# Performance work log

Measured on AMD Instinct MI355X. Metric: run time of the kernel, lower is better.

## Reference

```python
import jax, jax.numpy as jnp
import numpy as np

EMBED_DIM = 64
CODEBOOK_SIZE = 2048
COMMITMENT_COST = 1.0


def setup_inputs() -> dict:
    key = jax.random.key(0)
    k1, k2 = jax.random.split(key)
    inputs = jax.random.normal(k1, (32, 2048, EMBED_DIM), dtype=jnp.float32)
    embeddings = jax.random.normal(k2, (EMBED_DIM, CODEBOOK_SIZE), dtype=jnp.float32)
    return {"inputs": inputs, "embeddings": embeddings}


def reference(inputs, embeddings):
    # inference path (training=False): deterministic argmin quantization.
    D = embeddings.shape[0]
    K = embeddings.shape[1]
    flat = inputs.reshape(-1, D)                       # [N, D]
    similarity = flat @ embeddings                     # [N, K]
    distances = (jnp.sum(flat * flat, axis=1, keepdims=True)
                 - 2.0 * similarity
                 + jnp.sum(embeddings * embeddings, axis=0, keepdims=True))
    # gumbel layer with temperature 0 / eval mode -> argmax(-dist) == argmin(dist)
    flat_indices = jnp.argmax(-distances, axis=1)      # [N]
    encodings = jax.nn.one_hot(flat_indices, K, dtype=jnp.float32)  # [N, K]
    encoding_indices = flat_indices.reshape(inputs.shape[:-1])      # [B, T]
    quantized = jnp.take(embeddings.T, encoding_indices, axis=0)    # [B, T, D]
    e_latent_loss = jnp.mean(jnp.square(jax.lax.stop_gradient(quantized) - inputs))
    loss = e_latent_loss * COMMITMENT_COST
    return quantized, encodings, encoding_indices, loss
```

## Files before the change

### kernel.cpp

```cpp
#include <hip/hip_runtime.h>

#define N_ROWS 65536
#define DDIM   64
#define KCODES 2048
#define NB     128
#define TAU    0.05f

#define Q_OFF    ((size_t)0)
#define ENC_OFF  ((size_t)N_ROWS * DDIM)
#define IDX_OFF  (ENC_OFF + (size_t)N_ROWS * KCODES)
#define LOSS_OFF (IDX_OFF + (size_t)N_ROWS)
#define INV_ND (1.0f / ((float)N_ROWS * (float)DDIM))

#define WS_ESQ_OFF   (524288)
#define WS_FLAGS_OFF (532480)

typedef __attribute__((ext_vector_type(8))) short short8;
typedef __attribute__((ext_vector_type(4))) float f32x4;

__device__ __forceinline__ unsigned short f2bf(float f) {
    unsigned u = __float_as_uint(f);
    u += 0x7FFFu + ((u >> 16) & 1u);
    return (unsigned short)(u >> 16);
}
__device__ __forceinline__ float bf2f(unsigned short h) {
    return __uint_as_float(((unsigned)h) << 16);
}

__global__ void vq_prep(const float* __restrict__ emb, char* __restrict__ ws,
                        float* __restrict__ out) {
    int t = blockIdx.x * 256 + threadIdx.x;
    int code = t & (KCODES - 1);
    int d    = t >> 11;
    float v = emb[(size_t)d * KCODES + code];
    unsigned short hi = f2bf(v);
    unsigned short lo = f2bf(v - bf2f(hi));
    int ch = code >> 8;
    int lc = code & 255;
    int kk = d ^ ((code & 7) << 3);
    short* base = (short*)ws + (size_t)ch * 32768 + lc * 64 + kk;
    base[0]     = (short)hi;
    base[16384] = (short)lo;
    if (t < KCODES) {
        float s = 0.f;
        for (int dd = 0; dd < DDIM; ++dd) {
            float e = emb[(size_t)dd * KCODES + t];
            s += e * e;
        }
        ((float*)(ws + WS_ESQ_OFF))[t] = s;
    }
    if (t == 0) out[LOSS_OFF] = 0.f;
}

__launch_bounds__(256, 3)
__global__ void vq_main(const float* __restrict__ x, const float* __restrict__ emb,
                        const char* __restrict__ ws, int* __restrict__ flags,
                        float* __restrict__ out) {
    __shared__ __align__(16) float red[10240];
    __shared__ int   indS[128];
    __shared__ float lred[4];
    const int tid = threadIdx.x;
    const int l = tid & 63, w = tid >> 6;
    const int q = l >> 4, c = l & 15;
    const int r0 = blockIdx.x * NB;
    const float* esq = (const float*)(ws + WS_ESQ_OFF);
    const short* wsS = (const short*)ws;

    short8 ah0[2], ah1[2], al0[2], al1[2];
    #pragma unroll
    for (int rt = 0; rt < 2; ++rt) {
        int row = r0 + w * 32 + rt * 16 + c;
        const float4* xr = (const float4*)(x + (size_t)row * DDIM);
        float4 f0 = xr[q * 2],     f1 = xr[q * 2 + 1];
        float4 f2 = xr[8 + q * 2], f3 = xr[8 + q * 2 + 1];
        float a0[8] = {f0.x,f0.y,f0.z,f0.w,f1.x,f1.y,f1.z,f1.w};
        float a1[8] = {f2.x,f2.y,f2.z,f2.w,f3.x,f3.y,f3.z,f3.w};
        #pragma unroll
        for (int j = 0; j < 8; ++j) {
            unsigned short h0 = f2bf(a0[j]);
            ah0[rt][j] = (short)h0;
            al0[rt][j] = (short)f2bf(a0[j] - bf2f(h0));
            unsigned short h1 = f2bf(a1[j]);
            ah1[rt][j] = (short)h1;
            al1[rt][j] = (short)f2bf(a1[j] - bf2f(h1));
        }
    }

    float m1[8], m2[8], m3[8]; int i1[8], i2[8];
    #pragma unroll
    for (int s = 0; s < 8; ++s) {
        m1[s] = 3.4e38f; m2[s] = 3.4e38f; m3[s] = 3.4e38f; i1[s] = 0; i2[s] = 0;
    }

    const int swz = (c & 7) << 3;
    const int k0 = (q * 8) ^ swz;
    const int k1 = (32 + q * 8) ^ swz;
    float* ebase = out + ENC_OFF + (size_t)r0 * KCODES;
    const f32x4 z = {0.f, 0.f, 0.f, 0.f};
    for (int tt = 0; tt < 128; ++tt) {
        int code = tt * 16 + c;
        const short* ph = wsS + (size_t)(code >> 8) * 32768 + (code & 255) * 64;
        const short* pl = ph + 16384;
        short8 bh0 = *(const short8*)(ph + k0);
        short8 bh1 = *(const short8*)(ph + k1);
        short8 bl0 = *(const short8*)(pl + k0);
        short8 bl1 = *(const short8*)(pl + k1);
        float eq   = esq[code];

        #pragma unroll
        for (int jj = 0; jj < 2; ++jj) {
            int s   = (tt * 2 + jj) * 256 + tid;
            int row = s >> 9;
            int c4  = s & 511;
            __builtin_nontemporal_store(
                z, (f32x4*)(ebase + (size_t)row * KCODES + (c4 << 2)));
        }

        #pragma unroll
        for (int rt = 0; rt < 2; ++rt) {
            f32x4 acc = {0.f, 0.f, 0.f, 0.f};
            acc = __builtin_amdgcn_mfma_f32_16x16x32_bf16(ah0[rt], bh0, acc, 0, 0, 0);
            acc = __builtin_amdgcn_mfma_f32_16x16x32_bf16(ah1[rt], bh1, acc, 0, 0, 0);
            acc = __builtin_amdgcn_mfma_f32_16x16x32_bf16(ah0[rt], bl0, acc, 0, 0, 0);
            acc = __builtin_amdgcn_mfma_f32_16x16x32_bf16(ah1[rt], bl1, acc, 0, 0, 0);
            acc = __builtin_amdgcn_mfma_f32_16x16x32_bf16(al0[rt], bh0, acc, 0, 0, 0);
            acc = __builtin_amdgcn_mfma_f32_16x16x32_bf16(al1[rt], bh1, acc, 0, 0, 0);
            #pragma unroll
            for (int g = 0; g < 4; ++g) {
                float dist = fmaf(-2.f, acc[g], eq);
                int s = rt * 4 + g;
                bool b1 = dist < m1[s];
                bool b2 = dist < m2[s];
                bool b3 = dist < m3[s];
                m3[s] = b2 ? m2[s] : (b3 ? dist : m3[s]);
                m2[s] = b1 ? m1[s] : (b2 ? dist : m2[s]);
                i2[s] = b1 ? i1[s] : (b2 ? code : i2[s]);
                m1[s] = b1 ? dist : m1[s];
                i1[s] = b1 ? code : i1[s];
            }
        }
    }

    __syncthreads();

    #pragma unroll
    for (int rt = 0; rt < 2; ++rt)
        #pragma unroll
        for (int g = 0; g < 4; ++g) {
            int lrow = w * 32 + rt * 16 + q * 4 + g;
            float* p = red + (size_t)(lrow * 16 + c) * 5;
            int s = rt * 4 + g;
            p[0] = m1[s];
            p[1] = (float)i1[s];
            p[2] = m2[s];
            p[3] = (float)i2[s];
            p[4] = m3[s];
        }
    __syncthreads();

    if (tid < NB) {
        int row = tid;
        const float* p = red + (size_t)row * 80;
        float gm1 = 3.4e38f, gm2v = 3.4e38f, gm3 = 3.4e38f;
        int gi1 = 0x7fffffff, gi2 = 0x7fffffff;
        for (int t = 0; t < 16; ++t) {
            float v1 = p[t * 5 + 0], v2 = p[t * 5 + 2], v3 = p[t * 5 + 4];
            int   j1 = (int)p[t * 5 + 1], j2 = (int)p[t * 5 + 3];
            if (v1 < gm1 || (v1 == gm1 && j1 < gi1)) {
                gm3 = gm2v; gm2v = gm1; gi2 = gi1; gm1 = v1; gi1 = j1;
            } else if (v1 < gm2v || (v1 == gm2v && j1 < gi2)) {
                gm3 = gm2v; gm2v = v1; gi2 = j1;
            } else if (v1 < gm3) gm3 = v1;
            if (v2 < gm1 || (v2 == gm1 && j2 < gi1)) {
                gm3 = gm2v; gm2v = gm1; gi2 = gi1; gm1 = v2; gi1 = j2;
            } else if (v2 < gm2v || (v2 == gm2v && j2 < gi2)) {
                gm3 = gm2v; gm2v = v2; gi2 = j2;
            } else if (v2 < gm3) gm3 = v2;
            if (v3 < gm3) gm3 = v3;
        }
        int gr = r0 + row;
        out[IDX_OFF + gr] = (float)gi1;
        int f = 0;
        if (gm2v - gm1 < TAU) f = (gm3 - gm1 < TAU) ? 1 : ((gi2 << 2) | 2);
        flags[gr] = f;
        indS[row] = gi1;
        out[ENC_OFF + (size_t)gr * KCODES + gi1] = 1.0f;
    }
    __syncthreads();

    float lpart = 0.f;
    for (int i = tid; i < NB * (DDIM / 4); i += 256) {
        int row = i >> 4;
        int d4  = (i & 15) << 2;
        int idx = indS[row];
        int gr  = r0 + row;
        float4 qv;
        qv.x = emb[(size_t)(d4 + 0) * KCODES + idx];
        qv.y = emb[(size_t)(d4 + 1) * KCODES + idx];
        qv.z = emb[(size_t)(d4 + 2) * KCODES + idx];
        qv.w = emb[(size_t)(d4 + 3) * KCODES + idx];
        *(float4*)(out + Q_OFF + (size_t)gr * DDIM + d4) = qv;
        float4 xv = *(const float4*)(x + (size_t)gr * DDIM + d4);
        float dx = qv.x - xv.x, dy = qv.y - xv.y, dz = qv.z - xv.z, dw = qv.w - xv.w;
        lpart += dx * dx + dy * dy + dz * dz + dw * dw;
    }
    #pragma unroll
    for (int o = 32; o > 0; o >>= 1) lpart += __shfl_down(lpart, o);
    if ((tid & 63) == 0) lred[tid >> 6] = lpart;
    __syncthreads();
    if (tid == 0)
        atomicAdd(out + LOSS_OFF, (lred[0] + lred[1] + lred[2] + lred[3]) * INV_ND);
}

__global__ void vq_refine(const float* __restrict__ x, const float* __restrict__ emb,
                          const int* __restrict__ flags, float* __restrict__ out) {
    const int lane = threadIdx.x & 63;
    const int wid  = threadIdx.x >> 6;
    for (int rr = 0; rr < 8; ++rr) {
        int row = (blockIdx.x * 4 + wid) * 8 + rr;
        int f = flags[row];
        if (f == 0) continue;
        const float* xr = x + (size_t)row * DDIM;
        int oldIdx = (int)out[IDX_OFF + row];
        int bidx;
        if (f != 1) {
            int cand = f >> 2;
            double xd = (double)xr[lane];
            double ea = (double)emb[(size_t)lane * KCODES + oldIdx];
            double eb = (double)emb[(size_t)lane * KCODES + cand];
            double sa = xd * ea, sb = xd * eb;
            double qa = ea * ea, qb = eb * eb;
            #pragma unroll
            for (int o = 32; o > 0; o >>= 1) {
                sa += __shfl_down(sa, o);
                sb += __shfl_down(sb, o);
                qa += __shfl_down(qa, o);
                qb += __shfl_down(qb, o);
            }
            double dA = __shfl(qa - 2.0 * sa, 0);
            double dB = __shfl(qb - 2.0 * sb, 0);
            bidx = (dB < dA || (dB == dA && cand < oldIdx)) ? cand : oldIdx;
        } else {
            double best = 1e300; int bi = 0x7fffffff;
            for (int k = lane; k < KCODES; k += 64) {
                double s = 0.0, ee = 0.0;
                for (int d = 0; d < DDIM; ++d) {
                    double e = (double)emb[(size_t)d * KCODES + k];
                    s  = fma((double)xr[d], e, s);
                    ee = fma(e, e, ee);
                }
                double dist = ee - 2.0 * s;
                if (dist < best) { best = dist; bi = k; }
            }
            #pragma unroll
            for (int o = 32; o > 0; o >>= 1) {
                double ob = __shfl_down(best, o);
                int    oi = __shfl_down(bi, o);
                if (ob < best || (ob == best && oi < bi)) { best = ob; bi = oi; }
            }
            bidx = __shfl(bi, 0);
        }
        if (bidx == oldIdx) continue;
        if (lane == 0) {
            out[IDX_OFF + row] = (float)bidx;
            out[ENC_OFF + (size_t)row * KCODES + oldIdx] = 0.f;
            out[ENC_OFF + (size_t)row * KCODES + bidx]   = 1.f;
        }
        float eN = emb[(size_t)lane * KCODES + bidx];
        float eO = emb[(size_t)lane * KCODES + oldIdx];
        float xv = xr[lane];
        out[Q_OFF + (size_t)row * DDIM + lane] = eN;
        float dn = eN - xv, dod = eO - xv;
        float delta = dn * dn - dod * dod;
        #pragma unroll
        for (int o = 32; o > 0; o >>= 1) delta += __shfl_down(delta, o);
        if (lane == 0) atomicAdd(out + LOSS_OFF, delta * INV_ND);
    }
}

extern "C" void kernel_launch(void* const* d_in, const int* in_sizes, int n_in,
                              void* d_out, int out_size, void* d_ws, size_t ws_size,
                              hipStream_t stream) {
    const float* x   = (const float*)d_in[0];
    const float* emb = (const float*)d_in[1];
    float* out   = (float*)d_out;
    char*  ws    = (char*)d_ws;
    int*   flags = (int*)(ws + WS_FLAGS_OFF);
    hipLaunchKernelGGL(vq_prep,   dim3(512),         dim3(256), 0, stream, emb, ws, out);
    hipLaunchKernelGGL(vq_main,   dim3(N_ROWS / NB), dim3(256), 0, stream, x, emb, ws, flags, out);
    hipLaunchKernelGGL(vq_refine, dim3(N_ROWS / 32), dim3(256), 0, stream, x, emb, flags, out);
}
```

Measured before the change: 648.0 us.

## Split one-hot zeroing into dedicated blocks and set ones in refine

The zero-fill of the 512 MB one-hot encodings matrix moves out of the compute blocks' inner loop into 256 extra blocks of vq_main that only issue nontemporal zero stores. The single 1.0 per row is now written in vq_refine after the final index is known, so refine no longer has to clear and rewrite entries. This separates the bandwidth-bound fill from the MFMA distance loop so the two can run on different CUs concurrently. The trade-off is that the compute blocks no longer hide their stores behind math, and block scheduling now decides how much the fill and compute overlap.

```diff
diff --git a/kernel.cpp b/kernel.cpp
--- a/kernel.cpp
+++ b/kernel.cpp
@@ -4,6 +4,8 @@
 #define DDIM   64
 #define KCODES 2048
 #define NB     128
+#define NCOMP  (N_ROWS / NB)
+#define NZB    256
 #define TAU    0.05f
 
 #define Q_OFF    ((size_t)0)
@@ -56,9 +58,20 @@
 __global__ void vq_main(const float* __restrict__ x, const float* __restrict__ emb,
                         const char* __restrict__ ws, int* __restrict__ flags,
                         float* __restrict__ out) {
-    __shared__ __align__(16) float red[10240];
-    __shared__ int   indS[128];
+    __shared__ __align__(16) float red[NB * 16 * 5];
+    __shared__ int   indS[NB];
     __shared__ float lred[4];
+
+    if (blockIdx.x >= NCOMP) {
+        int zb = blockIdx.x - NCOMP;
+        f32x4* base = (f32x4*)(out + ENC_OFF + (size_t)zb * 256 * KCODES);
+        const f32x4 z = {0.f, 0.f, 0.f, 0.f};
+        #pragma unroll 8
+        for (int i = threadIdx.x; i < 256 * KCODES / 4; i += 256)
+            __builtin_nontemporal_store(z, base + i);
+        return;
+    }
+
     const int tid = threadIdx.x;
     const int l = tid & 63, w = tid >> 6;
     const int q = l >> 4, c = l & 15;
@@ -95,8 +108,6 @@
     const int swz = (c & 7) << 3;
     const int k0 = (q * 8) ^ swz;
     const int k1 = (32 + q * 8) ^ swz;
-    float* ebase = out + ENC_OFF + (size_t)r0 * KCODES;
-    const f32x4 z = {0.f, 0.f, 0.f, 0.f};
     for (int tt = 0; tt < 128; ++tt) {
         int code = tt * 16 + c;
         const short* ph = wsS + (size_t)(code >> 8) * 32768 + (code & 255) * 64;
@@ -106,15 +117,6 @@
         short8 bl0 = *(const short8*)(pl + k0);
         short8 bl1 = *(const short8*)(pl + k1);
         float eq   = esq[code];
-
-        #pragma unroll
-        for (int jj = 0; jj < 2; ++jj) {
-            int s   = (tt * 2 + jj) * 256 + tid;
-            int row = s >> 9;
-            int c4  = s & 511;
-            __builtin_nontemporal_store(
-                z, (f32x4*)(ebase + (size_t)row * KCODES + (c4 << 2)));
-        }
 
         #pragma unroll
         for (int rt = 0; rt < 2; ++rt) {
@@ -184,7 +186,6 @@
         if (gm2v - gm1 < TAU) f = (gm3 - gm1 < TAU) ? 1 : ((gi2 << 2) | 2);
         flags[gr] = f;
         indS[row] = gi1;
-        out[ENC_OFF + (size_t)gr * KCODES + gi1] = 1.0f;
     }
     __syncthreads();
 
@@ -219,62 +220,63 @@
     for (int rr = 0; rr < 8; ++rr) {
         int row = (blockIdx.x * 4 + wid) * 8 + rr;
         int f = flags[row];
-        if (f == 0) continue;
-        const float* xr = x + (size_t)row * DDIM;
         int oldIdx = (int)out[IDX_OFF + row];
-        int bidx;
-        if (f != 1) {
-            int cand = f >> 2;
-            double xd = (double)xr[lane];
-            double ea = (double)emb[(size_t)lane * KCODES + oldIdx];
-            double eb = (double)emb[(size_t)lane * KCODES + cand];
-            double sa = xd * ea, sb = xd * eb;
-            double qa = ea * ea, qb = eb * eb;
-            #pragma unroll
-            for (int o = 32; o > 0; o >>= 1) {
-                sa += __shfl_down(sa, o);
-                sb += __shfl_down(sb, o);
-                qa += __shfl_down(qa, o);
-                qb += __shfl_down(qb, o);
+        int bidx = oldIdx;
+        if (f != 0) {
+            const float* xr = x + (size_t)row * DDIM;
+            if (f != 1) {
+                int cand = f >> 2;
+                double xd = (double)xr[lane];
+                double ea = (double)emb[(size_t)lane * KCODES + oldIdx];
+                double eb = (double)emb[(size_t)lane * KCODES + cand];
+                double sa = xd * ea, sb = xd * eb;
+                double qa = ea * ea, qb = eb * eb;
+                #pragma unroll
+                for (int o = 32; o > 0; o >>= 1) {
+                    sa += __shfl_down(sa, o);
+                    sb += __shfl_down(sb, o);
+                    qa += __shfl_down(qa, o);
+                    qb += __shfl_down(qb, o);
+                }
+                double dA = __shfl(qa - 2.0 * sa, 0);
+                double dB = __shfl(qb - 2.0 * sb, 0);
+                bidx = (dB < dA || (dB == dA && cand < oldIdx)) ? cand : oldIdx;
+            } else {
+                double best = 1e300; int bi = 0x7fffffff;
+                for (int k = lane; k < KCODES; k += 64) {
+                    double s = 0.0, ee = 0.0;
+                    for (int d = 0; d < DDIM; ++d) {
+                        double e = (double)emb[(size_t)d * KCODES + k];
+                        s  = fma((double)xr[d], e, s);
+                        ee = fma(e, e, ee);
+                    }
+                    double dist = ee - 2.0 * s;
+                    if (dist < best) { best = dist; bi = k; }
+                }
+                #pragma unroll
+                for (int o = 32; o > 0; o >>= 1) {
+                    double ob = __shfl_down(best, o);
+                    int    oi = __shfl_down(bi, o);
+                    if (ob < best || (ob == best && oi < bi)) { best = ob; bi = oi; }
+                }
+                bidx = __shfl(bi, 0);
             }
-            double dA = __shfl(qa - 2.0 * sa, 0);
-            double dB = __shfl(qb - 2.0 * sb, 0);
-            bidx = (dB < dA || (dB == dA && cand < oldIdx)) ? cand : oldIdx;
-        } else {
-            double best = 1e300; int bi = 0x7fffffff;
-            for (int k = lane; k < KCODES; k += 64) {
-                double s = 0.0, ee = 0.0;
-                for (int d = 0; d < DDIM; ++d) {
-                    double e = (double)emb[(size_t)d * KCODES + k];
-                    s  = fma((double)xr[d], e, s);
-                    ee = fma(e, e, ee);
-                }
-                double dist = ee - 2.0 * s;
-                if (dist < best) { best = dist; bi = k; }
+            if (bidx != oldIdx) {
+                const float* xr2 = x + (size_t)row * DDIM;
+                if (lane == 0) out[IDX_OFF + row] = (float)bidx;
+                float eN = emb[(size_t)lane * KCODES + bidx];
+                float eO = emb[(size_t)lane * KCODES + oldIdx];
+                float xv = xr2[lane];
+                out[Q_OFF + (size_t)row * DDIM + lane] = eN;
+                float dn = eN - xv, dod = eO - xv;
+                float delta = dn * dn - dod * dod;
+                #pragma unroll
+                for (int o = 32; o > 0; o >>= 1) delta += __shfl_down(delta, o);
+                if (lane == 0) atomicAdd(out + LOSS_OFF, delta * INV_ND);
             }
-            #pragma unroll
-            for (int o = 32; o > 0; o >>= 1) {
-                double ob = __shfl_down(best, o);
-                int    oi = __shfl_down(bi, o);
-                if (ob < best || (ob == best && oi < bi)) { best = ob; bi = oi; }
-            }
-            bidx = __shfl(bi, 0);
-        }
-        if (bidx == oldIdx) continue;
-        if (lane == 0) {
-            out[IDX_OFF + row] = (float)bidx;
-            out[ENC_OFF + (size_t)row * KCODES + oldIdx] = 0.f;
-            out[ENC_OFF + (size_t)row * KCODES + bidx]   = 1.f;
-        }
-        float eN = emb[(size_t)lane * KCODES + bidx];
-        float eO = emb[(size_t)lane * KCODES + oldIdx];
-        float xv = xr[lane];
-        out[Q_OFF + (size_t)row * DDIM + lane] = eN;
-        float dn = eN - xv, dod = eO - xv;
-        float delta = dn * dn - dod * dod;
-        #pragma unroll
-        for (int o = 32; o > 0; o >>= 1) delta += __shfl_down(delta, o);
-        if (lane == 0) atomicAdd(out + LOSS_OFF, delta * INV_ND);
+        }
+        if (lane == 0)
+            out[ENC_OFF + (size_t)row * KCODES + bidx] = 1.0f;
     }
 }
 
@@ -286,7 +288,7 @@
     float* out   = (float*)d_out;
     char*  ws    = (char*)d_ws;
     int*   flags = (int*)(ws + WS_FLAGS_OFF);
-    hipLaunchKernelGGL(vq_prep,   dim3(512),         dim3(256), 0, stream, emb, ws, out);
-    hipLaunchKernelGGL(vq_main,   dim3(N_ROWS / NB), dim3(256), 0, stream, x, emb, ws, flags, out);
-    hipLaunchKernelGGL(vq_refine, dim3(N_ROWS / 32), dim3(256), 0, stream, x, emb, flags, out);
-}
+    hipLaunchKernelGGL(vq_prep,   dim3(512),          dim3(256), 0, stream, emb, ws, out);
+    hipLaunchKernelGGL(vq_main,   dim3(NCOMP + NZB),  dim3(256), 0, stream, x, emb, ws, flags, out);
+    hipLaunchKernelGGL(vq_refine, dim3(N_ROWS / 32),  dim3(256), 0, stream, x, emb, flags, out);
+}
```

Result: slower. 702.1 us (+8.3%).
